# Kernel optimization log

Measured on AMD Instinct MI355X. Metric: run time of the kernel, lower is better.

## Reference

```python
import jax, jax.numpy as jnp
import numpy as np

SCALE = 16.0
IGNORE_THRES = 0.5
NUM_CLASSES = 40
ANCHORS_PX = np.array([[16., 16.], [32., 32.], [64., 64.], [32., 64.], [64., 32.]], dtype=np.float32)
NB, NA, NH, NW, MAXT = 16, 5, 96, 96, 50


def setup_inputs() -> dict:
    key = jax.random.key(0)
    k1, k2, k3, k4, k5, k6, k7 = jax.random.split(key, 7)
    prediction = jax.random.normal(k1, (NB, NA, NH, NW, 5 + NUM_CLASSES), jnp.float32)
    # GT boxes in pixel space; x in [0, NW*SCALE), y in [0, NH*SCALE)
    xs = jax.random.uniform(k2, (NB, MAXT), minval=0.5, maxval=NW - 0.5) * SCALE
    ys = jax.random.uniform(k3, (NB, MAXT), minval=0.5, maxval=NH - 0.5) * SCALE
    hs = jax.random.uniform(k4, (NB, MAXT), minval=0.5, maxval=6.0) * SCALE
    ws = jax.random.uniform(k5, (NB, MAXT), minval=0.5, maxval=6.0) * SCALE
    lbl = jax.random.randint(k6, (NB, MAXT), 0, NUM_CLASSES)
    target = jnp.zeros((NB, MAXT, 13 + NUM_CLASSES), jnp.float32)
    target = target.at[..., 0].set(xs).at[..., 1].set(ys)
    target = target.at[..., 3].set(hs).at[..., 4].set(ws)  # source reads h from col 3, w from col 4
    target = target.at[..., 13:].set(jax.nn.one_hot(lbl, NUM_CLASSES, dtype=jnp.float32))
    target_sizes = jax.random.randint(k7, (NB,), 20, MAXT + 1)
    return {"prediction": prediction, "target": target, "target_sizes": target_sizes}


def _iou_xywh(g, p):
    # center/size boxes -> corners, with the original's +1 pixel convention
    g_x1, g_x2 = g[0] - g[2] / 2, g[0] + g[2] / 2
    g_y1, g_y2 = g[1] - g[3] / 2, g[1] + g[3] / 2
    p_x1, p_x2 = p[0] - p[2] / 2, p[0] + p[2] / 2
    p_y1, p_y2 = p[1] - p[3] / 2, p[1] + p[3] / 2
    iw = jnp.clip(jnp.minimum(g_x2, p_x2) - jnp.maximum(g_x1, p_x1) + 1., 0.)
    ih = jnp.clip(jnp.minimum(g_y2, p_y2) - jnp.maximum(g_y1, p_y1) + 1., 0.)
    inter = iw * ih
    ga = (g_x2 - g_x1 + 1.) * (g_y2 - g_y1 + 1.)
    pa = (p_x2 - p_x1 + 1.) * (p_y2 - p_y1 + 1.)
    return inter / (ga + pa - inter + 1e-16)


def _build_targets(pred_boxes, pred_conf, pred_cls, target, target_sizes, anchors):
    # Sequential scan over (batch, gt) preserves the torch double-loop's
    nB, nA, nH, nW = pred_conf.shape
    maxT = target.shape[1]
    aw, ah = anchors[:, 0], anchors[:, 1]
    anch_area = (aw + 1.) * (ah + 1.)
    mask = jnp.zeros((nB, nA, nH, nW), jnp.float32)
    conf_mask = jnp.ones((nB, nA, nH, nW), jnp.float32)
    tx = jnp.zeros_like(mask); ty = jnp.zeros_like(mask)
    tw = jnp.zeros_like(mask); th = jnp.zeros_like(mask)
    tconf = jnp.zeros_like(mask)
    tlabel = jnp.zeros((nB, nA, nH, nW), jnp.int32)  # argmax of one-hot tcls

    def step(carry, bt):
        mask, conf_mask, tx, ty, tw, th, tconf, tlabel, nGT, nCorrect = carry
        b = bt // maxT
        t = bt % maxT
        valid = t < target_sizes[b]
        row = target[b, t]
        gx = row[0] / SCALE; gy = row[1] / SCALE
        gw = row[4] / SCALE; gh = row[3] / SCALE  # w from col 4, h from col 3 (as in source)
        gi = gx.astype(jnp.int32); gj = gy.astype(jnp.int32)
        # anchor IoU: both boxes anchored at origin, corner-style with +1 (x1y1x2y2=True path)
        inter = jnp.clip(jnp.minimum(gw, aw) + 1., 0.) * jnp.clip(jnp.minimum(gh, ah) + 1., 0.)
        anch_ious = inter / ((gw + 1.) * (gh + 1.) + anch_area - inter + 1e-16)
        bd = jnp.where(valid, b, nB)  # out-of-bounds batch index -> scatter dropped when padded
        cur = conf_mask[b, :, gj, gi]
        conf_mask = conf_mask.at[bd, :, gj, gi].set(jnp.where(anch_ious > IGNORE_THRES, 0., cur), mode='drop')
        best_n = jnp.argmax(anch_ious)
        mask = mask.at[bd, best_n, gj, gi].set(1., mode='drop')
        conf_mask = conf_mask.at[bd, best_n, gj, gi].set(1., mode='drop')
        tx = tx.at[bd, best_n, gj, gi].set(gx - gi.astype(jnp.float32), mode='drop')
        ty = ty.at[bd, best_n, gj, gi].set(gy - gj.astype(jnp.float32), mode='drop')
        tw = tw.at[bd, best_n, gj, gi].set(jnp.log(gw / aw[best_n] + 1e-16), mode='drop')
        th = th.at[bd, best_n, gj, gi].set(jnp.log(gh / ah[best_n] + 1e-16), mode='drop')
        lbl = jnp.argmax(row[13:]).astype(jnp.int32)
        tlabel = tlabel.at[bd, best_n, gj, gi].set(lbl, mode='drop')
        tconf = tconf.at[bd, best_n, gj, gi].set(1., mode='drop')
        iou = _iou_xywh(jnp.stack([gx, gy, gw, gh]), pred_boxes[b, best_n, gj, gi])
        correct = valid & (iou > 0.5) & (jnp.argmax(pred_cls[b, best_n, gj, gi]) == lbl) & (pred_conf[b, best_n, gj, gi] > 0.5)
        return (mask, conf_mask, tx, ty, tw, th, tconf, tlabel,
                nGT + valid.astype(jnp.int32), nCorrect + correct.astype(jnp.int32)), None

    init = (mask, conf_mask, tx, ty, tw, th, tconf, tlabel,
            jnp.array(0, jnp.int32), jnp.array(0, jnp.int32))
    (mask, conf_mask, tx, ty, tw, th, tconf, tlabel, nGT, nCorrect), _ = jax.lax.scan(
        step, init, jnp.arange(nB * maxT))
    return mask, conf_mask, tx, ty, tw, th, tconf, tlabel, nGT, nCorrect


def _yolo_loss(prediction, target, target_sizes):
    nB, nA, nH, nW = prediction.shape[:4]
    pred_conf = prediction[..., 0]
    x = prediction[..., 1]; y = prediction[..., 2]
    h = prediction[..., 3]; w = prediction[..., 4]
    pred_cls = prediction[..., 5:]
    grid_x = jnp.arange(nW, dtype=jnp.float32).reshape(1, 1, 1, nW)
    grid_y = jnp.arange(nH, dtype=jnp.float32).reshape(1, 1, nH, 1)
    anchors = jnp.asarray(ANCHORS_PX) / SCALE  # grid units
    aw = anchors[:, 0].reshape(1, nA, 1, 1)
    ah = anchors[:, 1].reshape(1, nA, 1, 1)
    pred_boxes = jnp.stack([
        x + grid_x, y + grid_y, jnp.exp(w) * aw * jnp.ones_like(w), jnp.exp(h) * ah * jnp.ones_like(h)
    ], axis=-1)
    sg = jax.lax.stop_gradient  # torch uses .cpu().data inside build_targets
    mask, conf_mask, tx, ty, tw, th, tconf, tlabel, nGT, nCorrect = _build_targets(
        sg(pred_boxes), sg(pred_conf), sg(pred_cls), target, target_sizes, anchors)
    nM = jnp.sum(mask)
    mmean = lambda v: jnp.sum(mask * v) / nM  # masked MSE mean (size_average=True)
    loss_x = mmean((x - tx) ** 2)
    loss_y = mmean((y - ty) ** 2)
    loss_w = mmean((w - tw) ** 2)
    loss_h = mmean((h - th) ** 2)
    # BCEWithLogits, numerically stable
    bce = jnp.maximum(pred_conf, 0.) - pred_conf * tconf + jnp.log1p(jnp.exp(-jnp.abs(pred_conf)))
    # torch: conf_mask_false = (conf_mask - mask) as byte used as boolean mask -> nonzero selects
    cmf = (conf_mask != mask).astype(jnp.float32)
    loss_conf = jnp.sum(cmf * bce) / jnp.sum(cmf) + jnp.sum(mask * bce) / nM
    logp = jax.nn.log_softmax(pred_cls, axis=-1)
    ce = -jnp.take_along_axis(logp, tlabel[..., None], axis=-1)[..., 0]
    loss_cls = (1.0 / nB) * jnp.sum(mask * ce) / nM
    loss = loss_x + loss_y + loss_w + loss_h + loss_conf + loss_cls
    nProposals = jnp.sum(pred_conf > 0).astype(jnp.float32)
    recall = nCorrect.astype(jnp.float32) / jnp.maximum(nGT, 1).astype(jnp.float32)
    precision = jnp.where(nProposals > 0, nCorrect.astype(jnp.float32) / jnp.maximum(nProposals, 1.), 1.0)
    return (loss, loss_x + loss_y + loss_w + loss_h, loss_conf, loss_cls, recall, precision)


def reference(prediction, target, target_sizes):
    return _yolo_loss(prediction, target, target_sizes)
```

## Files before the change

kernel.cpp:

```cpp
#include <hip/hip_runtime.h>
#include <math.h>

#define NB 16
#define NA 5
#define NH 96
#define NW 96
#define MAXT 50
#define NC 40
#define CH 45
#define TGT_W 53
#define NCELL (NH*NW)
#define NTOT (NB*NA*NH*NW)
#define IGNORE_THRES 0.5f

#define CONFB 720

typedef float fvec4 __attribute__((ext_vector_type(4)));

__device__ __constant__ float c_AW[5] = {1.f, 2.f, 4.f, 2.f, 4.f};
__device__ __constant__ float c_AH[5] = {1.f, 2.f, 4.f, 4.f, 2.f};


__device__ __forceinline__ float softplusf(float p) {
    return fmaxf(p, 0.f) + log1pf(expf(-fabsf(p)));
}

__global__ __launch_bounds__(1024, 8) void fused(
    const float* __restrict__ pred, const float* __restrict__ tgt,
    const int* __restrict__ tsz, double* acc, int* corG, int* propI) {

    __shared__ int   s_key[MAXT], s_best[MAXT], s_ign[MAXT], s_lbl[MAXT];
    __shared__ float s_fx[MAXT], s_fy[MAXT], s_gw[MAXT], s_gh[MAXT];
    __shared__ int   s_cor[MAXT];
    __shared__ int   s_sl[MAXT * NA][6];
    __shared__ double red[16][9];
    __shared__ float sb[16];
    __shared__ int   sp[16];

    const int wave = threadIdx.x >> 6, lane = threadIdx.x & 63;

    if (blockIdx.x >= 16) {
        const int cb = blockIdx.x - 16;
        const unsigned cell = (unsigned)cb * 1024u + threadIdx.x;
        const unsigned fi = 45u * cell;
        const fvec4* __restrict__ p4 = (const fvec4*)pred;
        fvec4 v = p4[fi >> 2];
        const unsigned comp = fi & 3u;
        float p = (comp == 0u) ? v[0] : ((comp == 1u) ? v[1] : ((comp == 2u) ? v[2] : v[3]));

        float bce = softplusf(p);
        int prop = (p > 0.f) ? 1 : 0;

        #pragma unroll
        for (int off = 32; off; off >>= 1) {
            bce  += __shfl_down(bce, off);
            prop += __shfl_down(prop, off);
        }
        if (lane == 0) { sb[wave] = bce; sp[wave] = prop; }
        __syncthreads();
        if (threadIdx.x == 0) {
            float tb = 0.f; int tp = 0;
            #pragma unroll
            for (int w2 = 0; w2 < 16; ++w2) { tb += sb[w2]; tp += sp[w2]; }
            atomicAdd(&acc[0], (double)tb);
            atomicAdd(propI, tp);
        }
        return;
    }

    const int b = blockIdx.x;
    const int size_b = tsz[b];

    for (int t = wave; t < MAXT; t += 16) {
        const bool valid = t < size_b;
        const float* row = tgt + ((size_t)b * MAXT + t) * TGT_W;
        const float inv_s = 0.0625f;
        float gx = row[0] * inv_s, gy = row[1] * inv_s;
        float gh_ = row[3] * inv_s, gw_ = row[4] * inv_s;
        int gi = (int)gx, gj = (int)gy;

        float lv = (lane < NC) ? row[13 + lane] : -1e30f;
        int   li = (lane < NC) ? lane : (1 << 30);
        #pragma unroll
        for (int off = 32; off; off >>= 1) {
            float ov = __shfl_xor(lv, off);
            int   oi = __shfl_xor(li, off);
            if (ov > lv || (ov == lv && oi < li)) { lv = ov; li = oi; }
        }
        int lbl = li;

        float best_iou = -1e30f; int best = 0; int ign = 0;
        #pragma unroll
        for (int a = 0; a < 5; ++a) {
            float iw = fmaxf(fminf(gw_, c_AW[a]) + 1.f, 0.f);
            float ih = fmaxf(fminf(gh_, c_AH[a]) + 1.f, 0.f);
            float inter = iw * ih;
            float iou = inter / ((gw_ + 1.f) * (gh_ + 1.f) +
                                 (c_AW[a] + 1.f) * (c_AH[a] + 1.f) - inter + 1e-16f);
            if (iou > IGNORE_THRES) ign |= (1 << a);
            if (iou > best_iou) { best_iou = iou; best = a; }
        }

        size_t pbase = ((((size_t)b * NA + best) * NH + gj) * NW + gi) * CH;
        float pv = (lane < CH) ? pred[pbase + lane] : -1e30f;
        float pc = __shfl(pv, 0);
        float px = __shfl(pv, 1) + (float)gi;
        float py = __shfl(pv, 2) + (float)gj;
        float ph = expf(__shfl(pv, 3)) * c_AH[best];
        float pw = expf(__shfl(pv, 4)) * c_AW[best];

        float gx1 = gx - gw_ * 0.5f, gx2 = gx + gw_ * 0.5f;
        float gy1 = gy - gh_ * 0.5f, gy2 = gy + gh_ * 0.5f;
        float px1 = px - pw * 0.5f, px2 = px + pw * 0.5f;
        float py1 = py - ph * 0.5f, py2 = py + ph * 0.5f;
        float iw2 = fmaxf(fminf(gx2, px2) - fmaxf(gx1, px1) + 1.f, 0.f);
        float ih2 = fmaxf(fminf(gy2, py2) - fmaxf(gy1, py1) + 1.f, 0.f);
        float inter2 = iw2 * ih2;
        float ga = (gx2 - gx1 + 1.f) * (gy2 - gy1 + 1.f);
        float pa = (px2 - px1 + 1.f) * (py2 - py1 + 1.f);
        float iou2 = inter2 / (ga + pa - inter2 + 1e-16f);

        float cv = (lane >= 5 && lane < CH) ? pv : -1e30f;
        int   ci = (lane >= 5 && lane < CH) ? (lane - 5) : (1 << 30);
        #pragma unroll
        for (int off = 32; off; off >>= 1) {
            float ov = __shfl_xor(cv, off);
            int   oi = __shfl_xor(ci, off);
            if (ov > cv || (ov == cv && oi < ci)) { cv = ov; ci = oi; }
        }
        bool correct = valid && (iou2 > 0.5f) && (ci == lbl) && (pc > 0.5f);

        if (lane == 0) {
            s_key[t] = valid ? (gj * NW + gi) : -1;
            s_best[t] = best; s_ign[t] = ign; s_lbl[t] = lbl;
            s_fx[t] = gx - (float)gi; s_fy[t] = gy - (float)gj;
            s_gw[t] = gw_; s_gh[t] = gh_;
            s_cor[t] = correct ? 1 : 0;
        }
    }
    __syncthreads();

    if (threadIdx.x == 0) {
        int c = 0;
        for (int t = 0; t < MAXT; ++t) c += s_cor[t];
        corG[b] = c;
    }

    {
        const int t = threadIdx.x;
        if (t < MAXT) {
            const int myKey = s_key[t];
            bool owner = (myKey >= 0);
            if (owner)
                for (int u = t + 1; u < MAXT; ++u)
                    if (s_key[u] == myKey) { owner = false; break; }

            if (!owner) {
                #pragma unroll
                for (int a = 0; a < 5; ++a) s_sl[t * 5 + a][0] = 0;
            } else {
                int cm = 0x1F, m = 0;
                int w_[5] = {-1, -1, -1, -1, -1};
                for (int u = 0; u < MAXT; ++u) {
                    if (s_key[u] != myKey) continue;
                    cm &= ~s_ign[u];
                    int bn = s_best[u];
                    cm |= (1 << bn); m |= (1 << bn);
                    w_[bn] = u;
                }
                #pragma unroll
                for (int a = 0; a < 5; ++a) {
                    int* eSl = s_sl[t * 5 + a];
                    int ca = (b * NA + a) * NCELL + myKey;
                    int ma = (m >> a) & 1, cma = (cm >> a) & 1;
                    eSl[0] = ca | (ma << 20) | (cma << 21) | (1 << 22);
                    if (ma) {
                        int u = w_[a];
                        eSl[1] = s_lbl[u];
                        eSl[2] = __float_as_int(s_fx[u]);
                        eSl[3] = __float_as_int(s_fy[u]);
                        eSl[4] = __float_as_int(logf(s_gw[u] / c_AW[a] + 1e-16f));
                        eSl[5] = __float_as_int(logf(s_gh[u] / c_AH[a] + 1e-16f));
                    }
                }
            }
        }
    }
    __syncthreads();

    float loc[9];
    #pragma unroll
    for (int c = 0; c < 9; ++c) loc[c] = 0.f;

    for (int s = wave; s < MAXT * NA; s += 16) {
        int flags = s_sl[s][0];
        if (!(flags & (1 << 22))) continue;
        int ca = flags & 0xFFFFF;
        int ma = (flags >> 20) & 1, cma = (flags >> 21) & 1;
        size_t base = (size_t)ca * CH;
        float v = (lane < CH) ? pred[base + lane] : -1e30f;
        float p = __shfl(v, 0);
        float s0 = softplusf(p);
        int cmf = (cma != ma) ? 1 : 0;
        loc[0] += (cmf ? (s0 - p * (float)ma) : 0.f) - s0;
        loc[1] += (float)(cmf - 1);
        if (ma) {
            loc[2] += s0 - p;
            loc[8] += 1.f;
            float x = __shfl(v, 1), y = __shfl(v, 2);
            float hh = __shfl(v, 3), wv = __shfl(v, 4);
            float fx = __int_as_float(s_sl[s][2]), fy = __int_as_float(s_sl[s][3]);
            float tw_ = __int_as_float(s_sl[s][4]), th_ = __int_as_float(s_sl[s][5]);
            int lbl = s_sl[s][1];
            loc[4] += (x - fx) * (x - fx);
            loc[5] += (y - fy) * (y - fy);
            loc[6] += (wv - tw_) * (wv - tw_);
            loc[7] += (hh - th_) * (hh - th_);
            float cvv = (lane >= 5 && lane < CH) ? v : -1e30f;
            float mx = cvv;
            #pragma unroll
            for (int off = 32; off; off >>= 1) mx = fmaxf(mx, __shfl_xor(mx, off));
            float ex = (lane >= 5 && lane < CH) ? expf(v - mx) : 0.f;
            #pragma unroll
            for (int off = 32; off; off >>= 1) ex += __shfl_xor(ex, off);
            float cll = __shfl(v, 5 + lbl);
            loc[3] += logf(ex) + mx - cll;
        }
    }

    if (lane == 0) {
        #pragma unroll
        for (int c = 0; c < 9; ++c) red[wave][c] = (double)loc[c];
    }
    __syncthreads();
    if (threadIdx.x < 9) {
        double sum = 0.0;
        #pragma unroll
        for (int w2 = 0; w2 < 16; ++w2) sum += red[w2][threadIdx.x];
        if (sum != 0.0) atomicAdd(&acc[1 + threadIdx.x], sum);
    }
}

__global__ __launch_bounds__(64) void finalize(
    const double* __restrict__ acc, const int* __restrict__ corG,
    const int* __restrict__ tsz, const int* __restrict__ propI, float* out) {
    if (threadIdx.x != 0) return;
    int nCor = 0, nGT = 0;
    for (int b = 0; b < NB; ++b) { nCor += corG[b]; nGT += tsz[b]; }
    int nProp = *propI;

    double nM = acc[9];
    double inv_nM = 1.0 / (nM > 0.0 ? nM : 1e-16);
    double l_coord = (acc[5] + acc[6] + acc[7] + acc[8]) * inv_nM;
    double sum_cmf = (double)NTOT + acc[2];
    double l_conf = (acc[0] + acc[1]) / sum_cmf + acc[3] * inv_nM;
    double l_cls = (1.0 / (double)NB) * acc[4] * inv_nM;
    double loss = l_coord + l_conf + l_cls;
    float recall = (float)nCor / (float)(nGT > 1 ? nGT : 1);
    float precision = (nProp > 0) ? ((float)nCor / fmaxf((float)nProp, 1.f)) : 1.f;
    out[0] = (float)loss;
    out[1] = (float)l_coord;
    out[2] = (float)l_conf;
    out[3] = (float)l_cls;
    out[4] = recall;
    out[5] = precision;
}

extern "C" void kernel_launch(void* const* d_in, const int* in_sizes, int n_in,
                              void* d_out, int out_size, void* d_ws, size_t ws_size,
                              hipStream_t stream) {
    const float* pred = (const float*)d_in[0];
    const float* tgt  = (const float*)d_in[1];
    const int*   tsz  = (const int*)d_in[2];
    float* out = (float*)d_out;

    double* acc = (double*)d_ws;
    int* corG   = (int*)((char*)d_ws + 80);
    int* propI  = (int*)((char*)d_ws + 144);

    hipMemsetAsync(d_ws, 0, 160, stream);
    fused<<<16 + CONFB, 1024, 0, stream>>>(pred, tgt, tsz, acc, corG, propI);
    finalize<<<1, 64, 0, stream>>>(acc, corG, tsz, propI, out);
}
```

Measured before the change: 220.9 us.

## Spread conf-logit gather over 4 lanes per cell and replace atomics with partial sums

Each anchor cell's objectness logit is now read by four adjacent threads. Each loads a consecutive 16-byte chunk of an aligned 64-byte segment, and only the lane owning the logit contributes. The goal is wave-level loads that cover contiguous segments instead of scattered 16-byte accesses at a 180-byte stride. The grid grows fourfold. The per-block double and int atomics are replaced with per-block partial writes, which the finalize kernel reduces with 256 threads, removing atomic contention in exchange for an extra reduction pass.

```diff
diff --git a/kernel.cpp b/kernel.cpp
--- a/kernel.cpp
+++ b/kernel.cpp
@@ -13,13 +13,16 @@
 #define NTOT (NB*NA*NH*NW)
 #define IGNORE_THRES 0.5f
 
-#define CONFB 720
+#define CONFB 2880
 
 typedef float fvec4 __attribute__((ext_vector_type(4)));
 
 __device__ __constant__ float c_AW[5] = {1.f, 2.f, 4.f, 2.f, 4.f};
 __device__ __constant__ float c_AH[5] = {1.f, 2.f, 4.f, 4.f, 2.f};
 
+#define WS_CORG      80
+#define WS_PARTIAL_D 160
+#define WS_PARTIAL_I 23200
 
 __device__ __forceinline__ float softplusf(float p) {
     return fmaxf(p, 0.f) + log1pf(expf(-fabsf(p)));
@@ -27,7 +30,8 @@
 
 __global__ __launch_bounds__(1024, 8) void fused(
     const float* __restrict__ pred, const float* __restrict__ tgt,
-    const int* __restrict__ tsz, double* acc, int* corG, int* propI) {
+    const int* __restrict__ tsz, double* acc, int* corG,
+    double* partial_d, int* partial_i) {
 
     __shared__ int   s_key[MAXT], s_best[MAXT], s_ign[MAXT], s_lbl[MAXT];
     __shared__ float s_fx[MAXT], s_fy[MAXT], s_gw[MAXT], s_gh[MAXT];
@@ -41,15 +45,19 @@
 
     if (blockIdx.x >= 16) {
         const int cb = blockIdx.x - 16;
-        const unsigned cell = (unsigned)cb * 1024u + threadIdx.x;
-        const unsigned fi = 45u * cell;
+        const unsigned idx  = (unsigned)cb * 1024u + threadIdx.x;
+        const unsigned cell = idx >> 2, q = idx & 3u;
+        const unsigned fi   = 45u * cell;
+        const unsigned s4   = (fi >> 4) << 2;
         const fvec4* __restrict__ p4 = (const fvec4*)pred;
-        fvec4 v = p4[fi >> 2];
-        const unsigned comp = fi & 3u;
-        float p = (comp == 0u) ? v[0] : ((comp == 1u) ? v[1] : ((comp == 2u) ? v[2] : v[3]));
-
-        float bce = softplusf(p);
-        int prop = (p > 0.f) ? 1 : 0;
+        fvec4 v = p4[s4 + q];
+        const unsigned fis = fi & 15u;
+        const unsigned qc = fis >> 2, comp = fis & 3u;
+        float p = (comp == 0u) ? v[0] : ((comp == 1u) ? v[1]
+                  : ((comp == 2u) ? v[2] : v[3]));
+        const bool use = (q == qc);
+        float bce = use ? softplusf(p) : 0.f;
+        int  prop = (use && p > 0.f) ? 1 : 0;
 
         #pragma unroll
         for (int off = 32; off; off >>= 1) {
@@ -62,8 +70,8 @@
             float tb = 0.f; int tp = 0;
             #pragma unroll
             for (int w2 = 0; w2 < 16; ++w2) { tb += sb[w2]; tp += sp[w2]; }
-            atomicAdd(&acc[0], (double)tb);
-            atomicAdd(propI, tp);
+            partial_d[cb] = (double)tb;
+            partial_i[cb] = tp;
         }
         return;
     }
@@ -241,19 +249,35 @@
     }
 }
 
-__global__ __launch_bounds__(64) void finalize(
+__global__ __launch_bounds__(256) void finalize(
     const double* __restrict__ acc, const int* __restrict__ corG,
-    const int* __restrict__ tsz, const int* __restrict__ propI, float* out) {
+    const int* __restrict__ tsz,
+    const double* __restrict__ partial_d, const int* __restrict__ partial_i,
+    float* out) {
+    __shared__ double sd[256];
+    __shared__ int    si[256];
+    double db = 0.0; int ip = 0;
+    for (int i = threadIdx.x; i < CONFB; i += 256) { db += partial_d[i]; ip += partial_i[i]; }
+    sd[threadIdx.x] = db; si[threadIdx.x] = ip;
+    __syncthreads();
+    for (int off = 128; off; off >>= 1) {
+        if (threadIdx.x < off) {
+            sd[threadIdx.x] += sd[threadIdx.x + off];
+            si[threadIdx.x] += si[threadIdx.x + off];
+        }
+        __syncthreads();
+    }
     if (threadIdx.x != 0) return;
+    double sum_bce0 = sd[0];
+    int nProp = si[0];
     int nCor = 0, nGT = 0;
     for (int b = 0; b < NB; ++b) { nCor += corG[b]; nGT += tsz[b]; }
-    int nProp = *propI;
 
     double nM = acc[9];
     double inv_nM = 1.0 / (nM > 0.0 ? nM : 1e-16);
     double l_coord = (acc[5] + acc[6] + acc[7] + acc[8]) * inv_nM;
     double sum_cmf = (double)NTOT + acc[2];
-    double l_conf = (acc[0] + acc[1]) / sum_cmf + acc[3] * inv_nM;
+    double l_conf = (sum_bce0 + acc[1]) / sum_cmf + acc[3] * inv_nM;
     double l_cls = (1.0 / (double)NB) * acc[4] * inv_nM;
     double loss = l_coord + l_conf + l_cls;
     float recall = (float)nCor / (float)(nGT > 1 ? nGT : 1);
@@ -274,11 +298,13 @@
     const int*   tsz  = (const int*)d_in[2];
     float* out = (float*)d_out;
 
-    double* acc = (double*)d_ws;
-    int* corG   = (int*)((char*)d_ws + 80);
-    int* propI  = (int*)((char*)d_ws + 144);
+    double* acc       = (double*)d_ws;
+    int*    corG      = (int*)((char*)d_ws + WS_CORG);
+    double* partial_d = (double*)((char*)d_ws + WS_PARTIAL_D);
+    int*    partial_i = (int*)((char*)d_ws + WS_PARTIAL_I);
 
     hipMemsetAsync(d_ws, 0, 160, stream);
-    fused<<<16 + CONFB, 1024, 0, stream>>>(pred, tgt, tsz, acc, corG, propI);
-    finalize<<<1, 64, 0, stream>>>(acc, corG, tsz, propI, out);
+    fused<<<16 + CONFB, 1024, 0, stream>>>(pred, tgt, tsz, acc, corG,
+                                           partial_d, partial_i);
+    finalize<<<1, 256, 0, stream>>>(acc, corG, tsz, partial_d, partial_i, out);
 }
```

Measured after the change: 209.6 us. 1.05x faster.
